# Optimization experiments

Hardware: AMD Instinct MI355X
Metric: run time of the kernel (lower is better)

## Reference

```python
import jax, jax.numpy as jnp
import numpy as np

TEMPERATURE = 8.0  # sqrt(d_k), d_k = 64
MINIMUM_VALUE = -1e9  # stand-in for C.MINIMUM_VALUE


def setup_inputs() -> dict:
    key = jax.random.key(0)
    kq, kk, kv, km = jax.random.split(key, 4)
    B, N, D = 32, 2048, 64
    q = jax.random.normal(kq, (B, N, D), dtype=jnp.float32)
    k = jax.random.normal(kk, (B, N, D), dtype=jnp.float32)
    v = jax.random.normal(kv, (B, N, D), dtype=jnp.float32)
    mask = jax.random.randint(km, (B, N, N), 0, 2, dtype=jnp.int32)
    return {"q": q, "k": k, "v": v, "mask": mask}


def reference(q, k, v, mask):
    # scores: [B, Nq, Nk]
    attn = jnp.einsum("bqd,bkd->bqk", q, k) / TEMPERATURE
    attn = jnp.where(mask > 0, attn, MINIMUM_VALUE)
    attn = jax.nn.softmax(attn, axis=-1)
    # dropout is identity in eval / deterministic reference
    output = jnp.einsum("bqk,bkd->bqd", attn, v)
    return (output, attn)
```

## Files before the change

kernel.cpp:

```cpp
#include <hip/hip_runtime.h>

#define NB 32
#define NN 2048
#define ND 64
#define ROWS 16
#define NBLK (NB * NN / ROWS)

#define LDS_PART 65536
#define LDS_AUX  66048
#define LDS_TOTAL 70144

typedef _Float16 half8 __attribute__((ext_vector_type(8)));
typedef float f32x4 __attribute__((ext_vector_type(4)));
typedef int i32x4 __attribute__((ext_vector_type(4)));

union H4 { uint2 u; _Float16 h[4]; };

__device__ __forceinline__ f32x4 mfma16(half8 a, half8 b, f32x4 c) {
    return __builtin_amdgcn_mfma_f32_16x16x32_f16(a, b, c, 0, 0, 0);
}
#define SB() __builtin_amdgcn_sched_barrier(0)

__global__ __launch_bounds__(256) void cvt_f32_f16_k(const float* __restrict__ src,
                                                     _Float16* __restrict__ dst) {
    int i = blockIdx.x * 256 + threadIdx.x;
    const f32x4* s = (const f32x4*)src;
    f32x4 a = s[2 * i], b = s[2 * i + 1];
    half8 h;
    h[0] = (_Float16)a[0]; h[1] = (_Float16)a[1]; h[2] = (_Float16)a[2]; h[3] = (_Float16)a[3];
    h[4] = (_Float16)b[0]; h[5] = (_Float16)b[1]; h[6] = (_Float16)b[2]; h[7] = (_Float16)b[3];
    ((half8*)dst)[i] = h;
}

__global__ __launch_bounds__(256) void transpose_v_k(const float* __restrict__ v,
                                                     _Float16* __restrict__ vt) {
    __shared__ float tile[64][65];
    int b = blockIdx.x >> 5;
    int k0 = (blockIdx.x & 31) * 64;
    int t = threadIdx.x;
    {
        int dc = t & 15, kr = t >> 4;
        const f32x4* vp = (const f32x4*)(v + ((size_t)(b * NN + k0) * ND));
        #pragma unroll
        for (int i = 0; i < 4; ++i) {
            int kk = kr + i * 16;
            f32x4 x = vp[kk * 16 + dc];
            tile[kk][dc * 4 + 0] = x[0]; tile[kk][dc * 4 + 1] = x[1];
            tile[kk][dc * 4 + 2] = x[2]; tile[kk][dc * 4 + 3] = x[3];
        }
    }
    __syncthreads();
    {
        int d = t >> 2, ks = (t & 3) * 16;
        union { _Float16 hh[16]; uint4 u4[2]; } pk;
        #pragma unroll
        for (int j = 0; j < 16; ++j) pk.hh[j] = (_Float16)tile[ks + j][d];
        uint4* op = (uint4*)(vt + ((size_t)(b * ND + d) * NN + k0 + ks));
        op[0] = pk.u4[0]; op[1] = pk.u4[1];
    }
}

__global__ __launch_bounds__(256) void mask_pack_k(const int* __restrict__ mask,
                                                   unsigned long long* __restrict__ pm) {
    size_t gid = (size_t)blockIdx.x * 256 + threadIdx.x;
    size_t row = gid >> 5;
    int w = ((int)gid >> 2) & 7, lg = (int)gid & 3;
    const i32x4* mp = (const i32x4*)(mask + row * NN + w * 16 + lg * 4);
    unsigned long long bits = 0ull;
    #pragma unroll
    for (int i = 0; i < 16; i += 4) {
        i32x4 m0 = __builtin_nontemporal_load(mp + (size_t)(i + 0) * 32);
        i32x4 m1 = __builtin_nontemporal_load(mp + (size_t)(i + 1) * 32);
        i32x4 m2 = __builtin_nontemporal_load(mp + (size_t)(i + 2) * 32);
        i32x4 m3 = __builtin_nontemporal_load(mp + (size_t)(i + 3) * 32);
        unsigned b0 = (m0[0] > 0 ? 1u : 0u) | (m0[1] > 0 ? 2u : 0u) | (m0[2] > 0 ? 4u : 0u) | (m0[3] > 0 ? 8u : 0u);
        unsigned b1 = (m1[0] > 0 ? 1u : 0u) | (m1[1] > 0 ? 2u : 0u) | (m1[2] > 0 ? 4u : 0u) | (m1[3] > 0 ? 8u : 0u);
        unsigned b2 = (m2[0] > 0 ? 1u : 0u) | (m2[1] > 0 ? 2u : 0u) | (m2[2] > 0 ? 4u : 0u) | (m2[3] > 0 ? 8u : 0u);
        unsigned b3 = (m3[0] > 0 ? 1u : 0u) | (m3[1] > 0 ? 2u : 0u) | (m3[2] > 0 ? 4u : 0u) | (m3[3] > 0 ? 8u : 0u);
        bits |= (unsigned long long)(b0 | (b1 << 4) | (b2 << 8) | (b3 << 12)) << (i * 4);
    }
    pm[gid] = bits;
}

#define LDK(S, base) { \
    const _Float16* kk_ = kp + (size_t)(base) * (128 * ND); \
    S##0a = *(const half8*)(kk_);                S##0b = *(const half8*)(kk_ + 32); \
    S##1a = *(const half8*)(kk_ + 128 * ND);     S##1b = *(const half8*)(kk_ + 128 * ND + 32); \
    S##2a = *(const half8*)(kk_ + 2 * 128 * ND); S##2b = *(const half8*)(kk_ + 2 * 128 * ND + 32); \
    S##3a = *(const half8*)(kk_ + 3 * 128 * ND); S##3b = *(const half8*)(kk_ + 3 * 128 * ND + 32); }

#define CMP1(i, ka_, kb_) { \
    f32x4 acc = {0.f, 0.f, 0.f, 0.f}; \
    acc = mfma16(ka_, qf0, acc); \
    acc = mfma16(kb_, qf1, acc); \
    unsigned mb = (unsigned)(pmask >> ((i) * 4)) & 15u; \
    float e0 = (mb & 1u) ? __expf(acc[0] * 0.125f) : 0.f; \
    float e1 = (mb & 2u) ? __expf(acc[1] * 0.125f) : 0.f; \
    float e2 = (mb & 4u) ? __expf(acc[2] * 0.125f) : 0.f; \
    float e3 = (mb & 8u) ? __expf(acc[3] * 0.125f) : 0.f; \
    rsum += (e0 + e1) + (e2 + e3); \
    H4 y_; y_.h[0] = (_Float16)e0; y_.h[1] = (_Float16)e1; \
    y_.h[2] = (_Float16)e2; y_.h[3] = (_Float16)e3; \
    *(uint2*)(srow + ((((w * 16 + (i) * 128) + lg * 4) * 2) ^ sw)) = y_.u; }

#define CMP4(S, c) { CMP1((c)*4 + 0, S##0a, S##0b) CMP1((c)*4 + 1, S##1a, S##1b) \
                     CMP1((c)*4 + 2, S##2a, S##2b) CMP1((c)*4 + 3, S##3a, S##3b) }

#define LDV(S, base) { \
    const _Float16* vv_ = vp + (size_t)(kseg * 32 + (base)) * 32; \
    S##0 = *(const half8*)(vv_);       S##1 = *(const half8*)(vv_ + 32); \
    S##2 = *(const half8*)(vv_ + 64);  S##3 = *(const half8*)(vv_ + 96); \
    S##4 = *(const half8*)(vv_ + 128); S##5 = *(const half8*)(vv_ + 160); \
    S##6 = *(const half8*)(vv_ + 192); S##7 = *(const half8*)(vv_ + 224); }

#define PV1(ks_, vb_) { \
    half8 pa_ = *(const half8*)(pbase + ((((ks_) * 64) + lg * 16) ^ sw)); \
    o = mfma16(pa_, vb_, o); }

#define PV8(S, base) { PV1(kseg*32 + (base) + 0, S##0) PV1(kseg*32 + (base) + 1, S##1) \
                       PV1(kseg*32 + (base) + 2, S##2) PV1(kseg*32 + (base) + 3, S##3) \
                       PV1(kseg*32 + (base) + 4, S##4) PV1(kseg*32 + (base) + 5, S##5) \
                       PV1(kseg*32 + (base) + 6, S##6) PV1(kseg*32 + (base) + 7, S##7) }

#define NRM(jj) { \
    int colb_ = g * 8 + (jj) * 256; \
    H4 x_; x_.u = *(const uint2*)(s2 + (colb_ ^ sw2)); \
    f32x4 av_; \
    av_[0] = (float)x_.h[0] * linv; av_[1] = (float)x_.h[1] * linv; \
    av_[2] = (float)x_.h[2] * linv; av_[3] = (float)x_.h[3] * linv; \
    __builtin_nontemporal_store(av_, (f32x4*)(arow + (colb_ >> 1))); }

__global__ __launch_bounds__(512, 4) void attn_main_k(
        const _Float16* __restrict__ qh, const _Float16* __restrict__ kh,
        const _Float16* __restrict__ vtp, const unsigned long long* __restrict__ pm,
        float* __restrict__ outp, float* __restrict__ attnp) {
    extern __shared__ char smem[];

    int bid = blockIdx.x;
    int lin = (bid & 7) * (NBLK / 8) + (bid >> 3);
    int b  = lin >> 7;
    int q0 = (lin & 127) * ROWS;

    int t = threadIdx.x;
    int w = t >> 6, l = t & 63;
    int l15 = l & 15, lg = l >> 4;
    int sw = (l15 & 7) << 4;

    const _Float16* qb = qh + ((size_t)(b * NN + q0 + l15) * ND) + lg * 8;
    half8 qf0 = *(const half8*)(qb);
    half8 qf1 = *(const half8*)(qb + 32);

    unsigned long long pmask = pm[((size_t)(b * NN + q0 + l15) * 8 + w) * 4 + lg];

    const _Float16* kp = kh + (size_t)b * NN * ND + (size_t)(w * 16 + l15) * ND + lg * 8;
    char* srow = smem + l15 * 4096;

    half8 A0a, A0b, A1a, A1b, A2a, A2b, A3a, A3b;
    half8 B0a, B0b, B1a, B1b, B2a, B2b, B3a, B3b;
    float rsum = 0.f;
    LDK(A, 0)  SB();
    LDK(B, 4)  SB();
    CMP4(A, 0) SB();
    LDK(A, 8)  SB();
    CMP4(B, 1) SB();
    LDK(B, 12) SB();
    CMP4(A, 2) SB();
    CMP4(B, 3)

    rsum += __shfl_xor(rsum, 16);
    rsum += __shfl_xor(rsum, 32);
    float* part = (float*)(smem + LDS_PART);
    if (l < 16) part[w * 16 + l] = rsum;
    __syncthreads();

    {
        int r = t >> 5, g = t & 31;
        float su = 0.f;
        #pragma unroll
        for (int pw = 0; pw < 8; ++pw) su += part[pw * 16 + r];
        float linv = 1.0f / (su + 1e-37f);
        char* s2 = smem + r * 4096;
        int sw2 = (r & 7) << 4;
        float* arow = attnp + ((size_t)(b * NN + q0 + r)) * NN;
        NRM(0)  NRM(1)  NRM(2)  NRM(3)
        NRM(4)  NRM(5)  NRM(6)  NRM(7)
        NRM(8)  NRM(9)  NRM(10) NRM(11)
        NRM(12) NRM(13) NRM(14) NRM(15)
    }

    {
        int ct = w & 3, kseg = w >> 2;
        const _Float16* vp = vtp + (size_t)(b * ND + ct * 16 + l15) * NN + lg * 8;
        char* pbase = smem + l15 * 4096;
        f32x4 o = {0.f, 0.f, 0.f, 0.f};
        half8 V0, V1, V2, V3, V4, V5, V6, V7;
        half8 W0, W1, W2, W3, W4, W5, W6, W7;
        LDV(V, 0)   SB();
        LDV(W, 8)   SB();
        PV8(V, 0)   SB();
        LDV(V, 16)  SB();
        PV8(W, 8)   SB();
        LDV(W, 24)  SB();
        PV8(V, 16)  SB();
        PV8(W, 24)

        if (kseg) *(f32x4*)(smem + LDS_AUX + ((size_t)((w - 4) * 64 + l)) * 16) = o;
        __syncthreads();
        if (!kseg) {
            f32x4 o2 = *(const f32x4*)(smem + LDS_AUX + ((size_t)(w * 64 + l)) * 16);
            o += o2;
            float* ob = outp + ((size_t)(b * NN + q0 + lg * 4)) * ND + ct * 16 + l15;
            #pragma unroll
            for (int rr = 0; rr < 4; ++rr) {
                int qr = lg * 4 + rr;
                float s8 = 0.f;
                #pragma unroll
                for (int pw = 0; pw < 8; ++pw) s8 += part[pw * 16 + qr];
                __builtin_nontemporal_store(o[rr] / (s8 + 1e-37f), ob + (size_t)rr * ND);
            }
        }
    }
}

extern "C" void kernel_launch(void* const* d_in, const int* in_sizes, int n_in,
                              void* d_out, int out_size, void* d_ws, size_t ws_size,
                              hipStream_t stream) {
    const float* q = (const float*)d_in[0];
    const float* k = (const float*)d_in[1];
    const float* v = (const float*)d_in[2];
    const int* mask = (const int*)d_in[3];
    float* outp  = (float*)d_out;
    float* attnp = outp + (size_t)NB * NN * ND;

    _Float16* qh = (_Float16*)d_ws;
    _Float16* kh = qh + (size_t)NB * NN * ND;
    _Float16* vth = kh + (size_t)NB * NN * ND;
    unsigned long long* pm = (unsigned long long*)(vth + (size_t)NB * NN * ND);

    cvt_f32_f16_k<<<2048, 256, 0, stream>>>(q, qh);
    cvt_f32_f16_k<<<2048, 256, 0, stream>>>(k, kh);
    transpose_v_k<<<1024, 256, 0, stream>>>(v, vth);
    mask_pack_k<<<8192, 256, 0, stream>>>(mask, pm);
    attn_main_k<<<NBLK, 512, LDS_TOTAL, stream>>>(qh, kh, vth, pm, outp, attnp);
}
```

Baseline: 370.0 us.

## Specialize warps: half do PV matmul, half write normalized attention rows

Warps are split by role. Waves 0-3 compute the full P·V product over all keys, so the cross-wave LDS reduction and its second barrier are gone. Waves 4-7 normalize and store the attention matrix at the same time, using 16-byte LDS reads and two vector stores per lane. The aim is to overlap the heavy attention-output store traffic with the MFMA work and drop the LDS aux buffer, at the cost of a longer serial PV chain per wave and an uneven load between the two roles.

```diff
diff --git a/kernel.cpp b/kernel.cpp
--- a/kernel.cpp
+++ b/kernel.cpp
@@ -7,14 +7,14 @@
 #define NBLK (NB * NN / ROWS)
 
 #define LDS_PART 65536
-#define LDS_AUX  66048
-#define LDS_TOTAL 70144
+#define LDS_TOTAL 66048
 
 typedef _Float16 half8 __attribute__((ext_vector_type(8)));
 typedef float f32x4 __attribute__((ext_vector_type(4)));
 typedef int i32x4 __attribute__((ext_vector_type(4)));
 
 union H4 { uint2 u; _Float16 h[4]; };
+union H8 { uint4 u; _Float16 h[8]; };
 
 __device__ __forceinline__ f32x4 mfma16(half8 a, half8 b, f32x4 c) {
     return __builtin_amdgcn_mfma_f32_16x16x32_f16(a, b, c, 0, 0, 0);
@@ -107,7 +107,7 @@
                      CMP1((c)*4 + 2, S##2a, S##2b) CMP1((c)*4 + 3, S##3a, S##3b) }
 
 #define LDV(S, base) { \
-    const _Float16* vv_ = vp + (size_t)(kseg * 32 + (base)) * 32; \
+    const _Float16* vv_ = vp + (size_t)(base) * 32; \
     S##0 = *(const half8*)(vv_);       S##1 = *(const half8*)(vv_ + 32); \
     S##2 = *(const half8*)(vv_ + 64);  S##3 = *(const half8*)(vv_ + 96); \
     S##4 = *(const half8*)(vv_ + 128); S##5 = *(const half8*)(vv_ + 160); \
@@ -117,18 +117,21 @@
     half8 pa_ = *(const half8*)(pbase + ((((ks_) * 64) + lg * 16) ^ sw)); \
     o = mfma16(pa_, vb_, o); }
 
-#define PV8(S, base) { PV1(kseg*32 + (base) + 0, S##0) PV1(kseg*32 + (base) + 1, S##1) \
-                       PV1(kseg*32 + (base) + 2, S##2) PV1(kseg*32 + (base) + 3, S##3) \
-                       PV1(kseg*32 + (base) + 4, S##4) PV1(kseg*32 + (base) + 5, S##5) \
-                       PV1(kseg*32 + (base) + 6, S##6) PV1(kseg*32 + (base) + 7, S##7) }
+#define PV8(S, base) { PV1((base) + 0, S##0) PV1((base) + 1, S##1) \
+                       PV1((base) + 2, S##2) PV1((base) + 3, S##3) \
+                       PV1((base) + 4, S##4) PV1((base) + 5, S##5) \
+                       PV1((base) + 6, S##6) PV1((base) + 7, S##7) }
 
 #define NRM(jj) { \
-    int colb_ = g * 8 + (jj) * 256; \
-    H4 x_; x_.u = *(const uint2*)(s2 + (colb_ ^ sw2)); \
-    f32x4 av_; \
-    av_[0] = (float)x_.h[0] * linv; av_[1] = (float)x_.h[1] * linv; \
-    av_[2] = (float)x_.h[2] * linv; av_[3] = (float)x_.h[3] * linv; \
-    __builtin_nontemporal_store(av_, (f32x4*)(arow + (colb_ >> 1))); }
+    int colb_ = g * 16 + (jj) * 256; \
+    H8 x_; x_.u = *(const uint4*)(s2 + (colb_ ^ sw2)); \
+    f32x4 a0_, a1_; \
+    a0_[0] = (float)x_.h[0] * linv; a0_[1] = (float)x_.h[1] * linv; \
+    a0_[2] = (float)x_.h[2] * linv; a0_[3] = (float)x_.h[3] * linv; \
+    a1_[0] = (float)x_.h[4] * linv; a1_[1] = (float)x_.h[5] * linv; \
+    a1_[2] = (float)x_.h[6] * linv; a1_[3] = (float)x_.h[7] * linv; \
+    __builtin_nontemporal_store(a0_, (f32x4*)(arow + (colb_ >> 1))); \
+    __builtin_nontemporal_store(a1_, (f32x4*)(arow + (colb_ >> 1) + 4)); }
 
 __global__ __launch_bounds__(512, 4) void attn_main_k(
         const _Float16* __restrict__ qh, const _Float16* __restrict__ kh,
@@ -173,24 +176,8 @@
     if (l < 16) part[w * 16 + l] = rsum;
     __syncthreads();
 
-    {
-        int r = t >> 5, g = t & 31;
-        float su = 0.f;
-        #pragma unroll
-        for (int pw = 0; pw < 8; ++pw) su += part[pw * 16 + r];
-        float linv = 1.0f / (su + 1e-37f);
-        char* s2 = smem + r * 4096;
-        int sw2 = (r & 7) << 4;
-        float* arow = attnp + ((size_t)(b * NN + q0 + r)) * NN;
-        NRM(0)  NRM(1)  NRM(2)  NRM(3)
-        NRM(4)  NRM(5)  NRM(6)  NRM(7)
-        NRM(8)  NRM(9)  NRM(10) NRM(11)
-        NRM(12) NRM(13) NRM(14) NRM(15)
-    }
-
-    {
-        int ct = w & 3, kseg = w >> 2;
-        const _Float16* vp = vtp + (size_t)(b * ND + ct * 16 + l15) * NN + lg * 8;
+    if (w < 4) {
+        const _Float16* vp = vtp + (size_t)(b * ND + w * 16 + l15) * NN + lg * 8;
         char* pbase = smem + l15 * 4096;
         f32x4 o = {0.f, 0.f, 0.f, 0.f};
         half8 V0, V1, V2, V3, V4, V5, V6, V7;
@@ -202,23 +189,39 @@
         PV8(W, 8)   SB();
         LDV(W, 24)  SB();
         PV8(V, 16)  SB();
-        PV8(W, 24)
-
-        if (kseg) *(f32x4*)(smem + LDS_AUX + ((size_t)((w - 4) * 64 + l)) * 16) = o;
-        __syncthreads();
-        if (!kseg) {
-            f32x4 o2 = *(const f32x4*)(smem + LDS_AUX + ((size_t)(w * 64 + l)) * 16);
-            o += o2;
-            float* ob = outp + ((size_t)(b * NN + q0 + lg * 4)) * ND + ct * 16 + l15;
+        LDV(V, 32)  SB();
+        PV8(W, 24)  SB();
+        LDV(W, 40)  SB();
+        PV8(V, 32)  SB();
+        LDV(V, 48)  SB();
+        PV8(W, 40)  SB();
+        LDV(W, 56)  SB();
+        PV8(V, 48)  SB();
+        PV8(W, 56)
+
+        float* ob = outp + ((size_t)(b * NN + q0 + lg * 4)) * ND + w * 16 + l15;
+        #pragma unroll
+        for (int rr = 0; rr < 4; ++rr) {
+            int qr = lg * 4 + rr;
+            float s8 = 0.f;
             #pragma unroll
-            for (int rr = 0; rr < 4; ++rr) {
-                int qr = lg * 4 + rr;
-                float s8 = 0.f;
-                #pragma unroll
-                for (int pw = 0; pw < 8; ++pw) s8 += part[pw * 16 + qr];
-                __builtin_nontemporal_store(o[rr] / (s8 + 1e-37f), ob + (size_t)rr * ND);
-            }
+            for (int pw = 0; pw < 8; ++pw) s8 += part[pw * 16 + qr];
+            __builtin_nontemporal_store(o[rr] / (s8 + 1e-37f), ob + (size_t)rr * ND);
         }
+    } else {
+        int r = (w - 4) * 4 + lg;
+        int g = l15;
+        float su = 0.f;
+        #pragma unroll
+        for (int pw = 0; pw < 8; ++pw) su += part[pw * 16 + r];
+        float linv = 1.0f / (su + 1e-37f);
+        char* s2 = smem + r * 4096;
+        int sw2 = (r & 7) << 4;
+        float* arow = attnp + ((size_t)(b * NN + q0 + r)) * NN;
+        NRM(0)  NRM(1)  NRM(2)  NRM(3)
+        NRM(4)  NRM(5)  NRM(6)  NRM(7)
+        NRM(8)  NRM(9)  NRM(10) NRM(11)
+        NRM(12) NRM(13) NRM(14) NRM(15)
     }
 }
 
```

Result: slower. 418.3 us (+13.1%).
